# Kernel optimization log

Hardware: AMD Instinct MI355X
Metric: run time of the kernel (lower is better)

## Reference

```python
import jax, jax.numpy as jnp
import numpy as np

CUBOID = (2, 7, 7)
SHIFT = (1, 3, 3)
NUM_HEADS = 4
LN_EPS = 1e-5


def _cuboid_reorder(data, cs):
    # (B,T,H,W,C) -> (B, num_cuboids, cuboid_volume, C), strategy = ('l','l','l')
    B, T, H, W, C = data.shape
    bt, bh, bw = cs
    d = data.reshape(B, T // bt, bt, H // bh, bh, W // bw, bw, C)
    d = d.transpose(0, 1, 3, 5, 2, 4, 6, 7)
    return d.reshape(B, (T // bt) * (H // bh) * (W // bw), bt * bh * bw, C)


def _cuboid_reorder_reverse(data, cs, shape):
    T, H, W = shape
    bt, bh, bw = cs
    B, _, _, C = data.shape
    d = data.reshape(B, T // bt, H // bh, W // bw, bt, bh, bw, C)
    d = d.transpose(0, 1, 4, 2, 5, 3, 6, 7)
    return d.reshape(B, T, H, W, C)


def _compute_attn_mask(shape, cs, ss):
    # Shift-window mask; no padding needed (dims divisible by cuboid), so the
    # data mask is all-ones and the mask is just the shift-region equality mask.
    T, H, W = shape
    shift_mask = np.zeros((1, T, H, W, 1), np.float32)
    cnt = 0
    for t in (slice(-cs[0]), slice(-cs[0], -ss[0]), slice(-ss[0], None)):
        for h in (slice(-cs[1]), slice(-cs[1], -ss[1]), slice(-ss[1], None)):
            for w in (slice(-cs[2]), slice(-cs[2], -ss[2]), slice(-ss[2], None)):
                shift_mask[:, t, h, w, :] = cnt
                cnt += 1
    sm = _cuboid_reorder(shift_mask, cs)[0, :, :, 0]  # (num_cuboids, vol)
    attn_mask = (sm[:, None, :] - sm[:, :, None]) == 0  # (num_cuboids, vol, vol)
    return jnp.asarray(attn_mask)


def setup_inputs() -> dict:
    key = jax.random.key(0)
    k1, k2, k3 = jax.random.split(key, 3)
    B, T, H, W, C = 2, 16, 56, 56, 128
    return {
        "x": jax.random.normal(k1, (B, T, H, W, C), jnp.float32),
        "gamma": jnp.ones((C,), jnp.float32),
        "beta": jnp.zeros((C,), jnp.float32),
        "w_qkv": jax.random.normal(k2, (C, 3 * C), jnp.float32) * 0.05,
        "w_proj": jax.random.normal(k3, (C, C), jnp.float32) * 0.05,
        "b_proj": jnp.zeros((C,), jnp.float32),
    }


def reference(x, gamma, beta, w_qkv, w_proj, b_proj):
    B, T, H, W, C = x.shape
    hd = C // NUM_HEADS
    scale = hd ** -0.5

    # pre-norm (torch LayerNorm, biased variance)
    mu = jnp.mean(x, axis=-1, keepdims=True)
    var = jnp.var(x, axis=-1, keepdims=True)
    xn = (x - mu) * jax.lax.rsqrt(var + LN_EPS) * gamma + beta

    # shift + cuboid reorder
    shifted = jnp.roll(xn, shift=(-SHIFT[0], -SHIFT[1], -SHIFT[2]), axis=(1, 2, 3))
    r = _cuboid_reorder(shifted, CUBOID)  # (B, nc, vol, C)
    nc, vol = r.shape[1], r.shape[2]

    qkv = (r @ w_qkv).reshape(B, nc, vol, 3, NUM_HEADS, hd)
    q = qkv[..., 0, :, :] * scale  # (B, nc, vol, h, d)
    k = qkv[..., 1, :, :]
    v = qkv[..., 2, :, :]

    attn_score = jnp.einsum("bnihd,bnjhd->bhnij", q, k)  # (B, h, nc, vol, vol)
    mask = _compute_attn_mask((T, H, W), CUBOID, SHIFT)  # (nc, vol, vol)
    attn_score = jnp.where(mask[None, None], attn_score, jnp.float32(-1e18))
    attn = jax.nn.softmax(attn_score, axis=-1) * mask[None, None]

    out = jnp.einsum("bhnij,bnjhd->bnihd", attn, v).reshape(B, nc, vol, C)
    out = out @ w_proj + b_proj

    out = _cuboid_reorder_reverse(out, CUBOID, (T, H, W))
    out = jnp.roll(out, shift=SHIFT, axis=(1, 2, 3))
    return out
```

## Files before the change

### kernel.cpp

```cpp
#include <hip/hip_runtime.h>

typedef short s16x8 __attribute__((ext_vector_type(8)));
typedef float f32x4_t __attribute__((ext_vector_type(4)));

#define VOL 98
#define VPAD 112
#define CH 128
#define NWV 7
#define NTH (NWV * 64)
#define MASKNEG -1e9f

struct Smem {
  unsigned short bufA[VPAD * CH];
  unsigned short vt[CH * CH];
  unsigned short pst[NWV][512];
  unsigned int catbits[27][4];
  int cat[VPAD];
  int gidx[VPAD];
};

__device__ __forceinline__ unsigned short f2bf(float f) {
  unsigned int u = __float_as_uint(f);
  unsigned int r = u + 0x7FFFu + ((u >> 16) & 1u);
  return (unsigned short)(r >> 16);
}
__device__ __forceinline__ unsigned int pk2(float a, float b) {
#if __has_builtin(__builtin_amdgcn_perm)
  return __builtin_amdgcn_perm(__float_as_uint(b) + 0x8000u,
                               __float_as_uint(a) + 0x8000u,
                               0x07060302u);
#else
  return (unsigned int)f2bf(a) | ((unsigned int)f2bf(b) << 16);
#endif
}
__device__ __forceinline__ int swz(int row, int colEl, int strideB) {
  return (row * strideB + colEl * 2) ^ ((row & 7) << 4);
}
__device__ __forceinline__ s16x8 ldsRd(const unsigned short* buf, int row, int colEl, int strideB) {
  return *(const s16x8*)((const char*)buf + swz(row, colEl, strideB));
}
__device__ __forceinline__ void ldsWr64(unsigned short* buf, int row, int colEl, int strideB,
                                        unsigned int lo, unsigned int hi) {
  unsigned long long v = (unsigned long long)lo | ((unsigned long long)hi << 32);
  *(unsigned long long*)((char*)buf + swz(row, colEl, strideB)) = v;
}
__device__ __forceinline__ void ldsWr128(unsigned short* buf, int row, int colEl, int strideB, uint4 v) {
  *(uint4*)((char*)buf + swz(row, colEl, strideB)) = v;
}
__device__ __forceinline__ s16x8 u4cast(unsigned a, unsigned b, unsigned c, unsigned d) {
  union { uint4 u; s16x8 v; } cv;
  cv.u = make_uint4(a, b, c, d);
  return cv.v;
}

__global__ void prepack_weights(const float* __restrict__ wqkv,
                                const float* __restrict__ wproj,
                                unsigned short* __restrict__ dst) {
  int lane = threadIdx.x;
  int blk = blockIdx.x;
  if (blk < 96) {
    int ct = blk >> 2, ks = blk & 3;
    int r0 = ks * 32 + ((lane >> 4) << 3);
    int col = ct * 16 + (lane & 15);
    unsigned short* d = dst + (((size_t)(ct * 4 + ks) * 64 + lane) * 8);
#pragma unroll
    for (int j = 0; j < 8; ++j) d[j] = f2bf(wqkv[(size_t)(r0 + j) * 384 + col]);
  } else {
    int bb = blk - 96;
    int ct = bb >> 2, ks = bb & 3;
    int r0 = ks * 32 + ((lane >> 4) << 3);
    int col = ct * 16 + (lane & 15);
    unsigned short* d = dst + 49152 + (((size_t)(ct * 4 + ks) * 64 + lane) * 8);
#pragma unroll
    for (int j = 0; j < 8; ++j) d[j] = f2bf(wproj[(size_t)(r0 + j) * 128 + col]);
  }
}

__global__ __launch_bounds__(NTH, 4) void fused_cuboid_attn(
    const float* __restrict__ x, const float* __restrict__ gamma,
    const float* __restrict__ beta, const float* __restrict__ bproj,
    const unsigned short* __restrict__ wfrag, float* __restrict__ out) {
  __shared__ Smem s;
  const int tid = threadIdx.x;
  const int lane = tid & 63;
  const int itw = tid >> 6;
  const int l15 = lane & 15;
  const int lg = lane >> 4;
  const int lg4 = lg * 4;
  const int lg8 = lg * 8;
  const int bid = blockIdx.x;
  const int b = bid >> 9;
  const int n = bid & 511;
  const int nt = n >> 6, nh = (n >> 3) & 7, nw = n & 7;

  const int grp = tid >> 4;
  const int l = tid & 15;
  float4 xv[4][2];
  int giv[4], catv[4];
#pragma unroll
  for (int it2 = 0; it2 < 4; ++it2) {
    int i = grp + it2 * 28;
    if (i < VOL) {
      int dt = (i >= 49) ? 1 : 0;
      int rem = i - dt * 49;
      int dh = (rem * 37) >> 8;
      int dw = rem - dh * 7;
      int t = nt * 2 + dt, h = nh * 7 + dh, w = nw * 7 + dw;
      int ts = (t + 1) & 15;
      int hs = h + 3; if (hs >= 56) hs -= 56;
      int ws2 = w + 3; if (ws2 >= 56) ws2 -= 56;
      int gi = ((b * 16 + ts) * 56 + hs) * 56 + ws2;
      const float* xp = x + (size_t)gi * CH + l * 8;
      xv[it2][0] = *(const float4*)(xp);
      xv[it2][1] = *(const float4*)(xp + 4);
      giv[it2] = gi;
      int tc = (t < 14) ? 0 : ((t < 15) ? 1 : 2);
      int hc = (h < 49) ? 0 : ((h < 53) ? 1 : 2);
      int wc = (w < 49) ? 0 : ((w < 53) ? 1 : 2);
      catv[it2] = tc * 9 + hc * 3 + wc;
    }
  }

  {
    uint4 z = make_uint4(0, 0, 0, 0);
    uint4* pv = (uint4*)s.vt;
    for (int i = tid; i < 2048; i += NTH) pv[i] = z;
    if (tid < 224) ((uint4*)(s.bufA + 98 * CH))[tid] = z;
    if (tid < 27) ((uint4*)s.catbits)[tid] = z;
    if (tid >= NTH - (VPAD - VOL)) s.cat[VOL + tid - (NTH - (VPAD - VOL))] = -1;
  }
  __syncthreads();

  {
    const float4 g0 = *(const float4*)(gamma + l * 8);
    const float4 g1 = *(const float4*)(gamma + l * 8 + 4);
    const float4 be0 = *(const float4*)(beta + l * 8);
    const float4 be1 = *(const float4*)(beta + l * 8 + 4);
#pragma unroll
    for (int it2 = 0; it2 < 4; ++it2) {
      int i = grp + it2 * 28;
      if (i < VOL) {
        float4 v0 = xv[it2][0];
        float4 v1 = xv[it2][1];
        float sum = v0.x + v0.y + v0.z + v0.w + v1.x + v1.y + v1.z + v1.w;
        float ssq = v0.x * v0.x + v0.y * v0.y + v0.z * v0.z + v0.w * v0.w +
                    v1.x * v1.x + v1.y * v1.y + v1.z * v1.z + v1.w * v1.w;
#pragma unroll
        for (int d = 1; d < 16; d <<= 1) {
          sum += __shfl_xor(sum, d);
          ssq += __shfl_xor(ssq, d);
        }
        float mean = sum * (1.0f / 128.0f);
        float var = ssq * (1.0f / 128.0f) - mean * mean;
        float rstd = rsqrtf(var + 1e-5f);
        uint4 pkv;
        pkv.x = pk2((v0.x - mean) * rstd * g0.x + be0.x, (v0.y - mean) * rstd * g0.y + be0.y);
        pkv.y = pk2((v0.z - mean) * rstd * g0.z + be0.z, (v0.w - mean) * rstd * g0.w + be0.w);
        pkv.z = pk2((v1.x - mean) * rstd * g1.x + be1.x, (v1.y - mean) * rstd * g1.y + be1.y);
        pkv.w = pk2((v1.z - mean) * rstd * g1.z + be1.z, (v1.w - mean) * rstd * g1.w + be1.w);
        ldsWr128(s.bufA, i, l * 8, 256, pkv);
        if (l == 0) {
          s.cat[i] = catv[it2];
          s.gidx[i] = giv[it2];
          atomicOr(&s.catbits[catv[it2]][i >> 5], 1u << (i & 31));
        }
      }
    }
  }
  __syncthreads();

  s16x8 xf[4];
#pragma unroll
  for (int ks = 0; ks < 4; ++ks) xf[ks] = ldsRd(s.bufA, itw * 16 + l15, ks * 32 + lg8, 256);
  __syncthreads();

  unsigned qp[8][2];
  {
    const float QSCALE = (float)(0.17677669529663687 * 1.4426950408889634);
#pragma unroll
    for (int ct = 0; ct < 24; ++ct) {
      const unsigned short* wf = wfrag + ((size_t)ct * 2048 + (size_t)lane * 8);
      s16x8 wv[4];
#pragma unroll
      for (int ks = 0; ks < 4; ++ks) wv[ks] = *(const s16x8*)(wf + ks * 512);
      f32x4_t acc = {0.f, 0.f, 0.f, 0.f};
      if (ct < 16) {
#pragma unroll
        for (int ks = 0; ks < 4; ++ks)
          acc = __builtin_amdgcn_mfma_f32_16x16x32_bf16(wv[ks], xf[ks], acc, 0, 0, 0);
        if (ct < 8) {
          qp[ct][0] = pk2(acc[0] * QSCALE, acc[1] * QSCALE);
          qp[ct][1] = pk2(acc[2] * QSCALE, acc[3] * QSCALE);
        } else {
          ldsWr64(s.bufA, itw * 16 + l15, (ct - 8) * 16 + lg4, 256,
                  pk2(acc[0], acc[1]), pk2(acc[2], acc[3]));
        }
      } else {
#pragma unroll
        for (int ks = 0; ks < 4; ++ks)
          acc = __builtin_amdgcn_mfma_f32_16x16x32_bf16(xf[ks], wv[ks], acc, 0, 0, 0);
        ldsWr64(s.vt, (ct - 16) * 16 + l15, itw * 16 + lg4, 256,
                pk2(acc[0], acc[1]), pk2(acc[2], acc[3]));
      }
    }
  }
  __syncthreads();

  unsigned oreg[4][4];
  {
    unsigned short* ps = s.pst[itw];
    const int q = itw * 16 + l15;
    int cq = s.cat[q]; if (cq < 0) cq = 0;
    const uint4 mwv = *(const uint4*)&s.catbits[cq][0];
    f32x4_t cm[7];
#pragma unroll
    for (int jt = 0; jt < 7; ++jt) {
      unsigned mword = ((jt >> 1) == 0) ? mwv.x : ((jt >> 1) == 1) ? mwv.y
                      : ((jt >> 1) == 2) ? mwv.z : mwv.w;
#pragma unroll
      for (int r = 0; r < 4; ++r)
        cm[jt][r] = ((mword >> ((jt & 1) * 16 + lg4 + r)) & 1u) ? 0.f : MASKNEG;
    }
    const int srcA = ((lg & 1) * 2) * 16 + l15;
    const int srcB = ((lg & 1) * 2 + 1) * 16 + l15;
    const bool hiT = (lg >> 1) != 0;
#pragma unroll
    for (int hh = 0; hh < 4; ++hh) {
      unsigned a0 = __shfl(qp[2 * hh][0], srcA), b0 = __shfl(qp[2 * hh + 1][0], srcA);
      unsigned a1 = __shfl(qp[2 * hh][1], srcA), b1 = __shfl(qp[2 * hh + 1][1], srcA);
      unsigned a2 = __shfl(qp[2 * hh][0], srcB), b2 = __shfl(qp[2 * hh + 1][0], srcB);
      unsigned a3 = __shfl(qp[2 * hh][1], srcB), b3 = __shfl(qp[2 * hh + 1][1], srcB);
      s16x8 qa = u4cast(hiT ? b0 : a0, hiT ? b1 : a1, hiT ? b2 : a2, hiT ? b3 : a3);
      f32x4_t sc[7];
#pragma unroll
      for (int jt = 0; jt < 7; ++jt) {
        s16x8 kb = ldsRd(s.bufA, jt * 16 + l15, hh * 32 + lg8, 256);
        sc[jt] = __builtin_amdgcn_mfma_f32_16x16x32_bf16(kb, qa, cm[jt], 0, 0, 0);
      }
      float m0 = sc[0][0], m1 = sc[0][1], m2 = sc[0][2], m3 = sc[0][3];
#pragma unroll
      for (int jt = 1; jt < 7; ++jt) {
        m0 = fmaxf(m0, sc[jt][0]);
        m1 = fmaxf(m1, sc[jt][1]);
        m2 = fmaxf(m2, sc[jt][2]);
        m3 = fmaxf(m3, sc[jt][3]);
      }
      float m = fmaxf(fmaxf(m0, m1), fmaxf(m2, m3));
      m = fmaxf(m, __shfl_xor(m, 16));
      m = fmaxf(m, __shfl_xor(m, 32));
      float s0 = 0.f, s1 = 0.f, s2 = 0.f, s3 = 0.f;
#pragma unroll
      for (int jt = 0; jt < 7; ++jt) {
        float p0 = exp2f(sc[jt][0] - m);
        float p1 = exp2f(sc[jt][1] - m);
        float p2 = exp2f(sc[jt][2] - m);
        float p3 = exp2f(sc[jt][3] - m);
        sc[jt][0] = p0; sc[jt][1] = p1; sc[jt][2] = p2; sc[jt][3] = p3;
        s0 += p0; s1 += p1; s2 += p2; s3 += p3;
      }
      float ssum = (s0 + s1) + (s2 + s3);
      ssum += __shfl_xor(ssum, 16);
      ssum += __shfl_xor(ssum, 32);
      float rinv = 1.0f / ssum;
      f32x4_t o0 = {0.f, 0.f, 0.f, 0.f}, o1 = {0.f, 0.f, 0.f, 0.f};
#pragma unroll
      for (int ks = 0; ks < 4; ++ks) {
        const int jtA = 2 * ks, jtB = 2 * ks + 1;
        ldsWr64(ps, l15, lg4, 64, pk2(sc[jtA][0], sc[jtA][1]), pk2(sc[jtA][2], sc[jtA][3]));
        unsigned pb0 = 0, pb1 = 0;
        if (jtB < 7) {
          pb0 = pk2(sc[jtB][0], sc[jtB][1]);
          pb1 = pk2(sc[jtB][2], sc[jtB][3]);
        }
        ldsWr64(ps, l15, 16 + lg4, 64, pb0, pb1);
        asm volatile("" ::: "memory");
        s16x8 pa = ldsRd(ps, l15, lg8, 64);
        s16x8 v0 = ldsRd(s.vt, hh * 32 + l15, ks * 32 + lg8, 256);
        s16x8 v1 = ldsRd(s.vt, hh * 32 + 16 + l15, ks * 32 + lg8, 256);
        o0 = __builtin_amdgcn_mfma_f32_16x16x32_bf16(v0, pa, o0, 0, 0, 0);
        o1 = __builtin_amdgcn_mfma_f32_16x16x32_bf16(v1, pa, o1, 0, 0, 0);
      }
      oreg[hh][0] = pk2(o0[0] * rinv, o0[1] * rinv);
      oreg[hh][1] = pk2(o0[2] * rinv, o0[3] * rinv);
      oreg[hh][2] = pk2(o1[0] * rinv, o1[1] * rinv);
      oreg[hh][3] = pk2(o1[2] * rinv, o1[3] * rinv);
    }
  }
  __syncthreads();

  {
    const int q = itw * 16 + l15;
#pragma unroll
    for (int hh = 0; hh < 4; ++hh) {
      ldsWr64(s.bufA, q, hh * 32 + lg4, 256, oreg[hh][0], oreg[hh][1]);
      ldsWr64(s.bufA, q, hh * 32 + 16 + lg4, 256, oreg[hh][2], oreg[hh][3]);
    }
  }
  __syncthreads();

  {
    const unsigned short* wp = wfrag + 49152;
    s16x8 of[4];
#pragma unroll
    for (int ks = 0; ks < 4; ++ks) of[ks] = ldsRd(s.bufA, itw * 16 + l15, ks * 32 + lg8, 256);
    const int row = itw * 16 + l15;
    const bool valid = row < VOL;
    const size_t gbase = valid ? (size_t)s.gidx[row] * CH : 0;
#pragma unroll
    for (int ct = 0; ct < 8; ++ct) {
      const unsigned short* wf = wp + ((size_t)ct * 2048 + (size_t)lane * 8);
      float4 b4 = *(const float4*)(bproj + ct * 16 + lg4);
      f32x4_t acc = {b4.x, b4.y, b4.z, b4.w};
#pragma unroll
      for (int ks = 0; ks < 4; ++ks) {
        s16x8 wv = *(const s16x8*)(wf + ks * 512);
        acc = __builtin_amdgcn_mfma_f32_16x16x32_bf16(wv, of[ks], acc, 0, 0, 0);
      }
      if (valid) {
        float4 res;
        res.x = acc[0]; res.y = acc[1]; res.z = acc[2]; res.w = acc[3];
        *(float4*)(out + gbase + ct * 16 + lg4) = res;
      }
    }
  }
}

extern "C" void kernel_launch(void* const* d_in, const int* in_sizes, int n_in,
                              void* d_out, int out_size, void* d_ws, size_t ws_size,
                              hipStream_t stream) {
  const float* x = (const float*)d_in[0];
  const float* gamma = (const float*)d_in[1];
  const float* beta = (const float*)d_in[2];
  const float* wqkv = (const float*)d_in[3];
  const float* wproj = (const float*)d_in[4];
  const float* bproj = (const float*)d_in[5];
  float* out = (float*)d_out;
  unsigned short* wsf = (unsigned short*)d_ws;
  (void)in_sizes; (void)n_in; (void)out_size; (void)ws_size;

  prepack_weights<<<128, 64, 0, stream>>>(wqkv, wproj, wsf);
  fused_cuboid_attn<<<1024, NTH, 0, stream>>>(x, gamma, beta, bproj, wsf, out);
}
```

Measured before the change: 74.74 us.

## Compute V per head inside attention loop with double-buffered LDS, shuffle output

Moves the V projection out of the QKV prologue and computes it per head inside the attention loop, writing into a two-slot double-buffered LDS region sized for one head pair instead of a full 128x128 transposed V. The output-projection operand is now built from registers with cross-lane shuffles rather than an LDS round trip, which removes two block barriers. LDS use drops, but a block barrier is added inside every head iteration, and launch bounds go from 4 to 2 blocks per SM. This likely gives more registers per thread but may lower occupancy.

```diff
diff --git a/kernel.cpp b/kernel.cpp
--- a/kernel.cpp
+++ b/kernel.cpp
@@ -12,7 +12,7 @@
 
 struct Smem {
   unsigned short bufA[VPAD * CH];
-  unsigned short vt[CH * CH];
+  unsigned short vtH[2][32 * 128];
   unsigned short pst[NWV][512];
   unsigned int catbits[27][4];
   int cat[VPAD];
@@ -76,7 +76,7 @@
   }
 }
 
-__global__ __launch_bounds__(NTH, 4) void fused_cuboid_attn(
+__global__ __launch_bounds__(NTH, 2) void fused_cuboid_attn(
     const float* __restrict__ x, const float* __restrict__ gamma,
     const float* __restrict__ beta, const float* __restrict__ bproj,
     const unsigned short* __restrict__ wfrag, float* __restrict__ out) {
@@ -92,6 +92,9 @@
   const int b = bid >> 9;
   const int n = bid & 511;
   const int nt = n >> 6, nh = (n >> 3) & 7, nw = n & 7;
+  const int srcA = (2 * (lg & 1)) * 16 + l15;
+  const int srcB = (2 * (lg & 1) + 1) * 16 + l15;
+  const bool hiT = (lg >> 1) != 0;
 
   const int grp = tid >> 4;
   const int l = tid & 15;
@@ -123,8 +126,8 @@
 
   {
     uint4 z = make_uint4(0, 0, 0, 0);
-    uint4* pv = (uint4*)s.vt;
-    for (int i = tid; i < 2048; i += NTH) pv[i] = z;
+    uint4* pv = (uint4*)s.vtH;
+    for (int i = tid; i < 1024; i += NTH) pv[i] = z;
     if (tid < 224) ((uint4*)(s.bufA + 98 * CH))[tid] = z;
     if (tid < 27) ((uint4*)s.catbits)[tid] = z;
     if (tid >= NTH - (VPAD - VOL)) s.cat[VOL + tid - (NTH - (VPAD - VOL))] = -1;
@@ -178,28 +181,20 @@
   {
     const float QSCALE = (float)(0.17677669529663687 * 1.4426950408889634);
 #pragma unroll
-    for (int ct = 0; ct < 24; ++ct) {
+    for (int ct = 0; ct < 16; ++ct) {
       const unsigned short* wf = wfrag + ((size_t)ct * 2048 + (size_t)lane * 8);
       s16x8 wv[4];
 #pragma unroll
       for (int ks = 0; ks < 4; ++ks) wv[ks] = *(const s16x8*)(wf + ks * 512);
       f32x4_t acc = {0.f, 0.f, 0.f, 0.f};
-      if (ct < 16) {
-#pragma unroll
-        for (int ks = 0; ks < 4; ++ks)
-          acc = __builtin_amdgcn_mfma_f32_16x16x32_bf16(wv[ks], xf[ks], acc, 0, 0, 0);
-        if (ct < 8) {
-          qp[ct][0] = pk2(acc[0] * QSCALE, acc[1] * QSCALE);
-          qp[ct][1] = pk2(acc[2] * QSCALE, acc[3] * QSCALE);
-        } else {
-          ldsWr64(s.bufA, itw * 16 + l15, (ct - 8) * 16 + lg4, 256,
-                  pk2(acc[0], acc[1]), pk2(acc[2], acc[3]));
-        }
+#pragma unroll
+      for (int ks = 0; ks < 4; ++ks)
+        acc = __builtin_amdgcn_mfma_f32_16x16x32_bf16(wv[ks], xf[ks], acc, 0, 0, 0);
+      if (ct < 8) {
+        qp[ct][0] = pk2(acc[0] * QSCALE, acc[1] * QSCALE);
+        qp[ct][1] = pk2(acc[2] * QSCALE, acc[3] * QSCALE);
       } else {
-#pragma unroll
-        for (int ks = 0; ks < 4; ++ks)
-          acc = __builtin_amdgcn_mfma_f32_16x16x32_bf16(xf[ks], wv[ks], acc, 0, 0, 0);
-        ldsWr64(s.vt, (ct - 16) * 16 + l15, itw * 16 + lg4, 256,
+        ldsWr64(s.bufA, itw * 16 + l15, (ct - 8) * 16 + lg4, 256,
                 pk2(acc[0], acc[1]), pk2(acc[2], acc[3]));
       }
     }
@@ -221,11 +216,16 @@
       for (int r = 0; r < 4; ++r)
         cm[jt][r] = ((mword >> ((jt & 1) * 16 + lg4 + r)) & 1u) ? 0.f : MASKNEG;
     }
-    const int srcA = ((lg & 1) * 2) * 16 + l15;
-    const int srcB = ((lg & 1) * 2 + 1) * 16 + l15;
-    const bool hiT = (lg >> 1) != 0;
 #pragma unroll
     for (int hh = 0; hh < 4; ++hh) {
+      const unsigned short* wfV0 = wfrag + ((size_t)(16 + 2 * hh) * 2048 + (size_t)lane * 8);
+      const unsigned short* wfV1 = wfrag + ((size_t)(17 + 2 * hh) * 2048 + (size_t)lane * 8);
+      s16x8 wv0[4], wv1[4];
+#pragma unroll
+      for (int ks = 0; ks < 4; ++ks) {
+        wv0[ks] = *(const s16x8*)(wfV0 + ks * 512);
+        wv1[ks] = *(const s16x8*)(wfV1 + ks * 512);
+      }
       unsigned a0 = __shfl(qp[2 * hh][0], srcA), b0 = __shfl(qp[2 * hh + 1][0], srcA);
       unsigned a1 = __shfl(qp[2 * hh][1], srcA), b1 = __shfl(qp[2 * hh + 1][1], srcA);
       unsigned a2 = __shfl(qp[2 * hh][0], srcB), b2 = __shfl(qp[2 * hh + 1][0], srcB);
@@ -236,6 +236,17 @@
       for (int jt = 0; jt < 7; ++jt) {
         s16x8 kb = ldsRd(s.bufA, jt * 16 + l15, hh * 32 + lg8, 256);
         sc[jt] = __builtin_amdgcn_mfma_f32_16x16x32_bf16(kb, qa, cm[jt], 0, 0, 0);
+      }
+      {
+        f32x4_t aV0 = {0.f, 0.f, 0.f, 0.f}, aV1 = {0.f, 0.f, 0.f, 0.f};
+#pragma unroll
+        for (int ks = 0; ks < 4; ++ks) {
+          aV0 = __builtin_amdgcn_mfma_f32_16x16x32_bf16(xf[ks], wv0[ks], aV0, 0, 0, 0);
+          aV1 = __builtin_amdgcn_mfma_f32_16x16x32_bf16(xf[ks], wv1[ks], aV1, 0, 0, 0);
+        }
+        unsigned short* vh = s.vtH[hh & 1];
+        ldsWr64(vh, l15, itw * 16 + lg4, 256, pk2(aV0[0], aV0[1]), pk2(aV0[2], aV0[3]));
+        ldsWr64(vh, 16 + l15, itw * 16 + lg4, 256, pk2(aV1[0], aV1[1]), pk2(aV1[2], aV1[3]));
       }
       float m0 = sc[0][0], m1 = sc[0][1], m2 = sc[0][2], m3 = sc[0][3];
 #pragma unroll
@@ -262,6 +273,8 @@
       ssum += __shfl_xor(ssum, 16);
       ssum += __shfl_xor(ssum, 32);
       float rinv = 1.0f / ssum;
+      __syncthreads();
+      const unsigned short* vh = s.vtH[hh & 1];
       f32x4_t o0 = {0.f, 0.f, 0.f, 0.f}, o1 = {0.f, 0.f, 0.f, 0.f};
 #pragma unroll
       for (int ks = 0; ks < 4; ++ks) {
@@ -275,8 +288,8 @@
         ldsWr64(ps, l15, 16 + lg4, 64, pb0, pb1);
         asm volatile("" ::: "memory");
         s16x8 pa = ldsRd(ps, l15, lg8, 64);
-        s16x8 v0 = ldsRd(s.vt, hh * 32 + l15, ks * 32 + lg8, 256);
-        s16x8 v1 = ldsRd(s.vt, hh * 32 + 16 + l15, ks * 32 + lg8, 256);
+        s16x8 v0 = ldsRd(vh, l15, ks * 32 + lg8, 256);
+        s16x8 v1 = ldsRd(vh, 16 + l15, ks * 32 + lg8, 256);
         o0 = __builtin_amdgcn_mfma_f32_16x16x32_bf16(v0, pa, o0, 0, 0, 0);
         o1 = __builtin_amdgcn_mfma_f32_16x16x32_bf16(v1, pa, o1, 0, 0, 0);
       }
@@ -286,23 +299,18 @@
       oreg[hh][3] = pk2(o1[2] * rinv, o1[3] * rinv);
     }
   }
-  __syncthreads();
-
-  {
-    const int q = itw * 16 + l15;
+
+  {
+    s16x8 of[4];
 #pragma unroll
     for (int hh = 0; hh < 4; ++hh) {
-      ldsWr64(s.bufA, q, hh * 32 + lg4, 256, oreg[hh][0], oreg[hh][1]);
-      ldsWr64(s.bufA, q, hh * 32 + 16 + lg4, 256, oreg[hh][2], oreg[hh][3]);
-    }
-  }
-  __syncthreads();
-
-  {
+      unsigned a0 = __shfl(oreg[hh][0], srcA), a2 = __shfl(oreg[hh][2], srcA);
+      unsigned a1 = __shfl(oreg[hh][1], srcA), a3 = __shfl(oreg[hh][3], srcA);
+      unsigned c0 = __shfl(oreg[hh][0], srcB), c2 = __shfl(oreg[hh][2], srcB);
+      unsigned c1 = __shfl(oreg[hh][1], srcB), c3 = __shfl(oreg[hh][3], srcB);
+      of[hh] = u4cast(hiT ? a2 : a0, hiT ? a3 : a1, hiT ? c2 : c0, hiT ? c3 : c1);
+    }
     const unsigned short* wp = wfrag + 49152;
-    s16x8 of[4];
-#pragma unroll
-    for (int ks = 0; ks < 4; ++ks) of[ks] = ldsRd(s.bufA, itw * 16 + l15, ks * 32 + lg8, 256);
     const int row = itw * 16 + l15;
     const bool valid = row < VOL;
     const size_t gbase = valid ? (size_t)s.gidx[row] * CH : 0;
```

Result: slower. 90.20 us (+20.7%).
